# Kernel tuning notes

Hardware: AMD Instinct MI355X
Metric: run time of the kernel (lower is better)

Reference implementation:

```python
import jax, jax.numpy as jnp
import numpy as np

K = 20
EPS = 1e-5
SLOPE = 0.2


def _knn_idx(x, k):
    # x: [B, C, N] -> idx [B, N, k] of nearest neighbors by squared L2
    sq = jnp.sum(x * x, axis=1)                      # [B, N]
    inner = jnp.einsum('bcn,bcm->bnm', x, x)         # [B, N, N]
    neg_dist = 2.0 * inner - sq[:, :, None] - sq[:, None, :]
    return jax.lax.top_k(neg_dist, k)[1]             # [B, N, k]


def _edge_block(x, W, gamma, beta, k):
    # x: [B, C, N]; W: [O, 2C]; returns [B, O, N]
    idx = _knn_idx(x, k)
    xt = jnp.transpose(x, (0, 2, 1))                 # [B, N, C]
    nb = jax.vmap(lambda t, i: t[i])(xt, idx)        # [B, N, k, C] gather
    ctr = xt[:, :, None, :]
    edge = jnp.concatenate(
        [nb - ctr, jnp.broadcast_to(ctr, nb.shape)], axis=-1)  # [B, N, k, 2C]
    y = jnp.einsum('bnkc,oc->bonk', edge, W)         # 1x1 conv
    # BatchNorm2d (training mode: batch stats over B,N,k per channel)
    m = jnp.mean(y, axis=(0, 2, 3), keepdims=True)
    v = jnp.var(y, axis=(0, 2, 3), keepdims=True)
    y = (y - m) * jax.lax.rsqrt(v + EPS)
    y = y * gamma[None, :, None, None] + beta[None, :, None, None]
    y = jnp.where(y >= 0, y, SLOPE * y)              # LeakyReLU(0.2)
    return jnp.max(y, axis=-1)                       # max over k neighbors


def setup_inputs() -> dict:
    key = jax.random.key(0)
    ks = jax.random.split(key, 8)
    B, N = 8, 2048
    x = jax.random.normal(ks[0], (B, N, 3), dtype=jnp.float32)
    W1 = jax.random.normal(ks[1], (64, 6), dtype=jnp.float32) * 0.2
    W2 = jax.random.normal(ks[2], (128, 128), dtype=jnp.float32) * 0.08
    W3 = jax.random.normal(ks[3], (256, 256), dtype=jnp.float32) * 0.06
    g1, b1 = jnp.ones((64,), jnp.float32), jnp.zeros((64,), jnp.float32)
    g2, b2 = jnp.ones((128,), jnp.float32), jnp.zeros((128,), jnp.float32)
    g3, b3 = jnp.ones((256,), jnp.float32), jnp.zeros((256,), jnp.float32)
    L1 = jax.random.normal(ks[4], (1024, 448), dtype=jnp.float32) * 0.04
    L2 = jax.random.normal(ks[5], (2500, 1024), dtype=jnp.float32) * 0.03
    return {"x": x, "W1": W1, "g1": g1, "b1": b1, "W2": W2, "g2": g2,
            "b2": b2, "W3": W3, "g3": g3, "b3": b3, "L1": L1, "L2": L2}


def reference(x, W1, g1, b1, W2, g2, b2, W3, g3, b3, L1, L2):
    xT = jnp.transpose(x, (0, 2, 1))                 # [B, 3, N]
    x1 = _edge_block(xT, W1, g1, b1, K)              # [B, 64, N]
    x2 = _edge_block(x1, W2, g2, b2, K)              # [B, 128, N]
    x3 = _edge_block(x2, W3, g3, b3, K)              # [B, 256, N]
    feat = jnp.concatenate([x1, x2, x3], axis=1)     # [B, 448, N]
    pooled = jnp.max(feat, axis=-1)                  # adaptive_max_pool1d(1)
    h = pooled @ L1.T
    h = jnp.where(h >= 0, h, SLOPE * h)              # LeakyReLU(0.2)
    # dropout is identity in eval mode
    return h @ L2.T                                  # [B, 2500]
```

## Files before the change

kernel.cpp:

```cpp
#include <hip/hip_runtime.h>
#include <hip/hip_bf16.h>
#include <float.h>

#define K_NN 20
#define EPS 1e-5f
#define SLOPE 0.2f
constexpr int Bsz = 8;
constexpr int Npts = 2048;
constexpr int NQ = 8;
constexpr int BN = Bsz * Npts;

typedef __attribute__((ext_vector_type(8))) short short8v;
typedef __attribute__((ext_vector_type(4))) float f32x4;

__device__ __forceinline__ float dot4(float4 a, float4 b) {
  return a.x*b.x + a.y*b.y + a.z*b.z + a.w*b.w;
}
__device__ __forceinline__ unsigned encf(float f) {
  unsigned u = __float_as_uint(f);
  return (u & 0x80000000u) ? ~u : (u | 0x80000000u);
}
__device__ __forceinline__ float decf(unsigned e) {
  unsigned u = (e & 0x80000000u) ? (e & 0x7fffffffu) : ~e;
  return __uint_as_float(u);
}
__device__ __forceinline__ unsigned short f2bf(float x) {
  unsigned u = __float_as_uint(x);
  unsigned r = (u + 0x7fffu + ((u >> 16) & 1u)) >> 16;
  return (unsigned short)r;
}
__device__ __forceinline__ float bf2f(unsigned short h) {
  return __uint_as_float((unsigned)h << 16);
}
__device__ __forceinline__ f32x4 mfma16(short8v a, short8v b, f32x4 c) {
  return __builtin_amdgcn_mfma_f32_16x16x32_bf16(a, b, c, 0, 0, 0);
}

template<int C>
__global__ __launch_bounds__(256) void sq_kernel(const float* __restrict__ xt,
                                                 float* __restrict__ sq) {
  int p = blockIdx.x * 256 + threadIdx.x;
  if (p >= BN) return;
  const float* r = xt + (size_t)p * C;
  float s = 0.f;
  if constexpr (C % 4 == 0) {
    for (int c4 = 0; c4 < C / 4; ++c4) { float4 v = *(const float4*)(r + c4 * 4); s += dot4(v, v); }
  } else {
    #pragma unroll
    for (int c = 0; c < C; ++c) { float v = r[c]; s += v * v; }
  }
  sq[p] = s;
}

template<int C, int MT>
__global__ __launch_bounds__(256) void knn_part(const float* __restrict__ xt,
    const float* __restrict__ sq, float* __restrict__ pval, int* __restrict__ pidx) {
  constexpr int MQ = Npts / NQ;
  __shared__ __align__(16) float chk[MT][C];
  __shared__ float csq[MT];
  const int t = threadIdx.x, w = t >> 6, l = t & 63;
  const int rowblk = blockIdx.x / NQ;
  const int q = blockIdx.x - rowblk * NQ;
  const int p0 = rowblk * 256;
  const int b = p0 / Npts;
  const int myrow = p0 + w * 64 + l;

  float cr[C];
  #pragma unroll
  for (int c = 0; c < C; ++c) cr[c] = xt[(size_t)myrow * C + c];
  const float sqn = sq[myrow];

  float vals[K_NN]; int ids[K_NN];
  #pragma unroll
  for (int i = 0; i < K_NN; ++i) { vals[i] = -FLT_MAX; ids[i] = 0; }

  const int mbase = q * MQ;
  for (int m0 = mbase; m0 < mbase + MQ; m0 += MT) {
    __syncthreads();
    const float* s2 = xt + ((size_t)b * Npts + m0) * C;
    for (int e = t; e < MT * C; e += 256) chk[e / C][e - (e / C) * C] = s2[e];
    for (int e = t; e < MT; e += 256) csq[e] = sq[b * Npts + m0 + e];
    __syncthreads();
    for (int j = 0; j < MT; ++j) {
      float dt = 0.f;
      #pragma unroll
      for (int c = 0; c < C; ++c) dt += cr[c] * chk[j][c];
      float nd = 2.f * dt - sqn - csq[j];
      if (nd > vals[K_NN - 1]) {
        vals[K_NN - 1] = nd; ids[K_NN - 1] = m0 + j;
        #pragma unroll
        for (int i = K_NN - 1; i >= 1; --i) {
          if (vals[i] > vals[i - 1]) {
            float tv = vals[i]; vals[i] = vals[i-1]; vals[i-1] = tv;
            int ti = ids[i]; ids[i] = ids[i-1]; ids[i-1] = ti;
          }
        }
      }
    }
  }
  size_t base = ((size_t)q * BN + myrow) * K_NN;
  #pragma unroll
  for (int i = 0; i < K_NN; ++i) { pval[base + i] = vals[i]; pidx[base + i] = ids[i]; }
}

template<int NQM>
__global__ __launch_bounds__(256) void knn_merge(const float* __restrict__ pval,
    const int* __restrict__ pidx, int* __restrict__ idxout) {
  int p = blockIdx.x * 256 + threadIdx.x;
  if (p >= BN) return;
  float vals[K_NN]; int ids[K_NN];
  size_t base = (size_t)p * K_NN;
  #pragma unroll
  for (int i = 0; i < K_NN; ++i) { vals[i] = pval[base + i]; ids[i] = pidx[base + i]; }
  #pragma unroll
  for (int q = 1; q < NQM; ++q) {
    size_t b2 = ((size_t)q * BN + p) * K_NN;
    #pragma unroll
    for (int i = 0; i < K_NN; ++i) {
      float v = pval[b2 + i];
      if (v <= vals[K_NN - 1]) break;
      int m = pidx[b2 + i];
      vals[K_NN - 1] = v; ids[K_NN - 1] = m;
      #pragma unroll
      for (int r = K_NN - 1; r >= 1; --r) {
        if (vals[r] > vals[r - 1]) {
          float tv = vals[r]; vals[r] = vals[r-1]; vals[r-1] = tv;
          int ti = ids[r]; ids[r] = ids[r-1]; ids[r-1] = ti;
        }
      }
    }
  }
  int* op = idxout + (size_t)p * K_NN;
  #pragma unroll
  for (int i = 0; i < K_NN; ++i) op[i] = ids[i];
}

template<int C>
__global__ __launch_bounds__(256) void knn_fused(
    const unsigned short* __restrict__ xh, const unsigned short* __restrict__ xl,
    const float* __restrict__ sq, float* __restrict__ pval, int* __restrict__ pidx) {
  constexpr int KS = C / 32;
  constexpr int TPW = 4;
  __shared__ __align__(16) char smem[4 * 64 * 17 * 4];
  float (*dist)[64][17] = (float(*)[64][17])smem;
  float (*svv)[16][K_NN] = (float(*)[16][K_NN])smem;
  int   (*sii)[16][K_NN] = (int(*)[16][K_NN])(smem + 4 * 16 * K_NN * 4);
  const int bid = blockIdx.x;
  const int b = bid >> 8;
  const int rem = bid & 255;
  const int qt = rem >> 1, h = rem & 1;
  const int q0 = qt * 16;
  const int t = threadIdx.x, wv = t >> 6, l = t & 63, l15 = l & 15, grp = l >> 4;
  const unsigned short* xbh = xh + (size_t)b * Npts * C;
  const unsigned short* xbl = xl + (size_t)b * Npts * C;
  const float* sqb = sq + b * Npts;
  const int qi = q0 + l15;

  short8v bh[KS], bl[KS];
  #pragma unroll
  for (int ks = 0; ks < KS; ++ks) {
    const size_t a = (size_t)qi * C + ks * 32 + grp * 8;
    bh[ks] = *(const short8v*)(xbh + a);
    bl[ks] = *(const short8v*)(xbl + a);
  }
  const float sqn = sqb[qi];

  float vals[K_NN]; int ids[K_NN];
  #pragma unroll
  for (int i = 0; i < K_NN; ++i) { vals[i] = -FLT_MAX; ids[i] = 0; }

  #pragma unroll 1
  for (int ti = 0; ti < TPW; ++ti) {
    const int m0 = h * 1024 + (wv * TPW + ti) * 64;
    f32x4 acc[4];
    #pragma unroll
    for (int rt = 0; rt < 4; ++rt) acc[rt] = (f32x4){0.f, 0.f, 0.f, 0.f};
    #pragma unroll
    for (int ks = 0; ks < KS; ++ks) {
      #pragma unroll
      for (int rt = 0; rt < 4; ++rt) {
        const size_t aoff = (size_t)(m0 + rt * 16 + l15) * C + ks * 32 + grp * 8;
        const short8v a_h = *(const short8v*)(xbh + aoff);
        const short8v a_l = *(const short8v*)(xbl + aoff);
        acc[rt] = mfma16(a_h, bh[ks], acc[rt]);
        acc[rt] = mfma16(a_l, bh[ks], acc[rt]);
        acc[rt] = mfma16(a_h, bl[ks], acc[rt]);
      }
    }
    #pragma unroll
    for (int rt = 0; rt < 4; ++rt) {
      const int cb = m0 + rt * 16 + grp * 4;
      const float4 s4 = *(const float4*)(sqb + cb);
      const float sv[4] = {s4.x, s4.y, s4.z, s4.w};
      #pragma unroll
      for (int r = 0; r < 4; ++r) {
        const int cand = cb + r;
        float v = 2.f * acc[rt][r] - sqn - sv[r];
        if (cand == qi) v = 0.f;
        dist[wv][rt * 16 + grp * 4 + r][l15] = v;
      }
    }
    asm volatile("s_waitcnt lgkmcnt(0)" ::: "memory");
    __builtin_amdgcn_sched_barrier(0);
    #pragma unroll 4
    for (int j = 0; j < 16; ++j) {
      const float v = dist[wv][grp * 16 + j][l15];
      if (v > vals[K_NN - 1]) {
        const int cand = m0 + grp * 16 + j;
        vals[K_NN - 1] = v; ids[K_NN - 1] = cand;
        #pragma unroll
        for (int i = K_NN - 1; i >= 1; --i) {
          if (vals[i] > vals[i - 1]) {
            float tv = vals[i]; vals[i] = vals[i-1]; vals[i-1] = tv;
            int ti2 = ids[i]; ids[i] = ids[i-1]; ids[i-1] = ti2;
          }
        }
      }
    }
  }

  #pragma unroll
  for (int s2 = 1; s2 < 4; ++s2) {
    float ov[K_NN]; int oi[K_NN];
    #pragma unroll
    for (int i = 0; i < K_NN; ++i) {
      ov[i] = __shfl(vals[i], s2 * 16 + l15);
      oi[i] = __shfl(ids[i],  s2 * 16 + l15);
    }
    if (grp == 0) {
      #pragma unroll
      for (int i = 0; i < K_NN; ++i) {
        const float v = ov[i];
        if (v <= vals[K_NN - 1]) break;
        vals[K_NN - 1] = v; ids[K_NN - 1] = oi[i];
        #pragma unroll
        for (int r = K_NN - 1; r >= 1; --r) {
          if (vals[r] > vals[r - 1]) {
            float tv = vals[r]; vals[r] = vals[r-1]; vals[r-1] = tv;
            int ti2 = ids[r]; ids[r] = ids[r-1]; ids[r-1] = ti2;
          }
        }
      }
    }
  }
  __syncthreads();
  if (grp == 0) {
    #pragma unroll
    for (int i = 0; i < K_NN; ++i) { svv[wv][l15][i] = vals[i]; sii[wv][l15][i] = ids[i]; }
  }
  __syncthreads();
  if (t < 16) {
    #pragma unroll
    for (int s2 = 1; s2 < 4; ++s2) {
      #pragma unroll
      for (int i = 0; i < K_NN; ++i) {
        const float v = svv[s2][t][i];
        if (v <= vals[K_NN - 1]) break;
        vals[K_NN - 1] = v; ids[K_NN - 1] = sii[s2][t][i];
        #pragma unroll
        for (int r = K_NN - 1; r >= 1; --r) {
          if (vals[r] > vals[r - 1]) {
            float tv = vals[r]; vals[r] = vals[r-1]; vals[r-1] = tv;
            int ti2 = ids[r]; ids[r] = ids[r-1]; ids[r-1] = ti2;
          }
        }
      }
    }
    size_t base = ((size_t)h * BN + b * Npts + q0 + t) * K_NN;
    #pragma unroll
    for (int i = 0; i < K_NN; ++i) { pval[base + i] = vals[i]; pidx[base + i] = ids[i]; }
  }
}

template<int C, int O>
__global__ __launch_bounds__(256) void prep_w(const float* __restrict__ W,
    unsigned short* __restrict__ wh, unsigned short* __restrict__ wl) {
  int i = blockIdx.x * 256 + threadIdx.x;
  if (i >= 2 * O * C) return;
  int j = i / C, c = i - j * C;
  float v = (j < O) ? W[(size_t)j * 2 * C + c]
                    : (W[(size_t)(j - O) * 2 * C + C + c] - W[(size_t)(j - O) * 2 * C + c]);
  unsigned short h = f2bf(v);
  wh[i] = h; wl[i] = f2bf(v - bf2f(h));
}

template<int C, int N2>
__global__ __launch_bounds__(256) void zgemm(
    const unsigned short* __restrict__ xh, const unsigned short* __restrict__ xl,
    const unsigned short* __restrict__ wh, const unsigned short* __restrict__ wl,
    float* __restrict__ Z, int r0) {
  constexpr int KS = C / 32;
  constexpr int CB = N2 / 64;
  const int nb = blockIdx.x / CB, cb = blockIdx.x - nb * CB;
  const int ln0 = nb * 64;
  const int t = threadIdx.x, l = t & 63, wv = t >> 6, l15 = l & 15, grp = l >> 4;
  const int col = cb * 64 + wv * 16 + l15;
  f32x4 acc[4];
  #pragma unroll
  for (int rt = 0; rt < 4; ++rt) acc[rt] = (f32x4){0.f, 0.f, 0.f, 0.f};
  #pragma unroll
  for (int ks = 0; ks < KS; ++ks) {
    const int krd = ks * 32 + grp * 8;
    const short8v bh = *(const short8v*)(wh + (size_t)col * C + krd);
    const short8v bl = *(const short8v*)(wl + (size_t)col * C + krd);
    #pragma unroll
    for (int rt = 0; rt < 4; ++rt) {
      const size_t arow = (size_t)(r0 + ln0 + rt * 16 + l15) * C + krd;
      const short8v a_h = *(const short8v*)(xh + arow);
      const short8v a_l = *(const short8v*)(xl + arow);
      acc[rt] = mfma16(a_h, bh, acc[rt]);
      acc[rt] = mfma16(a_l, bh, acc[rt]);
      acc[rt] = mfma16(a_h, bl, acc[rt]);
    }
  }
  #pragma unroll
  for (int rt = 0; rt < 4; ++rt)
    #pragma unroll
    for (int r = 0; r < 4; ++r)
      Z[(size_t)(ln0 + rt * 16 + grp * 4 + r) * N2 + col] = acc[rt][r];
}

template<int O, int NPP>
__global__ __launch_bounds__(256) void nbr_reduce(
    const float* __restrict__ Z, const int* __restrict__ idx,
    float* __restrict__ mx, float* __restrict__ mn,
    float* __restrict__ psum, float* __restrict__ psq, int r0) {
  constexpr int PPB = 256 / O;
  constexpr int O2 = 2 * O;
  const int t = threadIdx.x;
  const int o = t % O;
  const int sub = t / O;
  float ls = 0.f, lq = 0.f;
  for (int it = 0; it < NPP / PPB; ++it) {
    const int p = r0 + blockIdx.x * NPP + it * PPB + sub;
    const int bbase = (p >> 11) << 11;
    const int* ip = idx + (size_t)p * K_NN;
    const float base = Z[(size_t)(p - r0) * O2 + O + o];
    float vmx = -FLT_MAX, vmn = FLT_MAX;
    #pragma unroll
    for (int k = 0; k < K_NN; ++k) {
      const int nbrow = bbase + ip[k] - r0;
      const float y = Z[(size_t)nbrow * O2 + o] + base;
      ls += y; lq = fmaf(y, y, lq);
      vmx = fmaxf(vmx, y); vmn = fminf(vmn, y);
    }
    mx[(size_t)p * O + o] = vmx;
    mn[(size_t)p * O + o] = vmn;
  }
  if constexpr (PPB > 1) {
    __shared__ float s1[256], s2[256];
    s1[t] = ls; s2[t] = lq;
    __syncthreads();
    if (sub == 0) {
      psum[(size_t)blockIdx.x * O + o] = ls + s1[t + O];
      psq [(size_t)blockIdx.x * O + o] = lq + s2[t + O];
    }
  } else {
    psum[(size_t)blockIdx.x * O + o] = ls;
    psq [(size_t)blockIdx.x * O + o] = lq;
  }
}

template<int C, int O, int G, int NPG, int CPT>
__global__ __launch_bounds__(256) void edge_kernel(const float* __restrict__ xt,
    const int* __restrict__ idx, const float* __restrict__ W,
    float* __restrict__ mx, float* __restrict__ mn,
    float* __restrict__ psum, float* __restrict__ psq) {
  constexpr int WP = O / (64 * CPT);
  constexpr int TPB = 64 * WP * NPG;
  constexpr int PPG = G / NPG;
  static_assert(TPB == 256, "block must be 256 threads");
  __shared__ __align__(16) float pts[G][K_NN + 1][C];
  __shared__ int ids[G][K_NN + 1];
  __shared__ float shps[NPG][O];
  __shared__ float shpq[NPG][O];
  const int t = threadIdx.x;
  const int p0 = blockIdx.x * G;
  const int b = p0 / Npts;

  for (int e = t; e < G * (K_NN + 1); e += TPB) {
    int g = e / (K_NN + 1), j = e - g * (K_NN + 1);
    ids[g][j] = (j == 0) ? (p0 + g) : (b * Npts + idx[(size_t)(p0 + g) * K_NN + (j - 1)]);
  }
  __syncthreads();
  for (int e = t; e < G * (K_NN + 1) * C; e += TPB) {
    int g = e / ((K_NN + 1) * C), rem = e - g * ((K_NN + 1) * C);
    int j = rem / C, c = rem - j * C;
    pts[g][j][c] = xt[(size_t)ids[g][j] * C + c];
  }
  __syncthreads();

  const int w = t >> 6, l = t & 63;
  const int pg = w / WP, wp = w - pg * WP;
  const int o0 = wp * 64 + l;
  float ls0 = 0.f, lq0 = 0.f;

  for (int it = 0; it < PPG; ++it) {
    const int g = pg * PPG + it;
    float yk0[K_NN];
    float u0 = 0.f, v0 = 0.f;
    #pragma unroll
    for (int k = 0; k < K_NN; ++k) yk0[k] = 0.f;
    const float* W0 = W + (size_t)o0 * (2 * C);
    #pragma unroll
    for (int c = 0; c < C; ++c) {
      const float wl = W0[c], whv = W0[C + c], ccv = pts[g][0][c];
      u0 += wl * ccv; v0 += whv * ccv;
      #pragma unroll
      for (int k = 0; k < K_NN; ++k) yk0[k] += wl * pts[g][k + 1][c];
    }
    const int n = p0 + g - b * Npts;
    const size_t obase = ((size_t)b * Npts + n) * O;
    const float base = v0 - u0;
    float vmx = -FLT_MAX, vmn = FLT_MAX;
    #pragma unroll
    for (int k = 0; k < K_NN; ++k) {
      float y = yk0[k] + base;
      ls0 += y; lq0 += y * y;
      vmx = fmaxf(vmx, y); vmn = fminf(vmn, y);
    }
    mx[obase + o0] = vmx; mn[obase + o0] = vmn;
  }

  shps[pg][o0] = ls0; shpq[pg][o0] = lq0;
  __syncthreads();
  if (t < O) {
    float s = 0.f, qq = 0.f;
    #pragma unroll
    for (int i = 0; i < NPG; ++i) { s += shps[i][t]; qq += shpq[i][t]; }
    psum[(size_t)blockIdx.x * O + t] = s;
    psq [(size_t)blockIdx.x * O + t] = qq;
  }
}

template<int O, int NBLK>
__global__ __launch_bounds__(256) void stats_part(const float* __restrict__ psum,
    const float* __restrict__ psq, double* __restrict__ pp, double* __restrict__ pq) {
  constexpr int NS = 16;
  constexpr int SL = NBLK / NS;
  const int l = threadIdx.x & 63, w = threadIdx.x >> 6;
  const int os = blockIdx.x % (O / 64), sl = blockIdx.x / (O / 64);
  const int o = os * 64 + l;
  double s = 0.0, ss = 0.0;
  for (int i = sl * SL + w; i < (sl + 1) * SL; i += 4) {
    s  += (double)psum[(size_t)i * O + o];
    ss += (double)psq [(size_t)i * O + o];
  }
  __shared__ double sh[2][4][64];
  sh[0][w][l] = s; sh[1][w][l] = ss;
  __syncthreads();
  if (w == 0) {
    s  = sh[0][0][l] + sh[0][1][l] + sh[0][2][l] + sh[0][3][l];
    ss = sh[1][0][l] + sh[1][1][l] + sh[1][2][l] + sh[1][3][l];
    pp[(size_t)sl * O + o] = s;
    pq[(size_t)sl * O + o] = ss;
  }
}

template<int O>
__global__ __launch_bounds__(64) void stats_final(const double* __restrict__ pp,
    const double* __restrict__ pq,
    const float* __restrict__ gamma, const float* __restrict__ beta,
    float* __restrict__ scale, float* __restrict__ bias) {
  const int o = blockIdx.x * 64 + threadIdx.x;
  double s = 0.0, ss = 0.0;
  #pragma unroll
  for (int sl = 0; sl < 16; ++sl) { s += pp[(size_t)sl * O + o]; ss += pq[(size_t)sl * O + o]; }
  double cnt = (double)Bsz * Npts * K_NN;
  double m = s / cnt;
  double var = ss / cnt - m * m;
  float g = gamma[o];
  float sc = g * rsqrtf((float)var + EPS);
  scale[o] = sc;
  bias[o] = beta[o] - (float)m * sc;
}

__global__ __launch_bounds__(256) void reset_pool(unsigned* __restrict__ pooled) {
  int i = blockIdx.x * 256 + threadIdx.x;
  if (i < Bsz * 448) pooled[i] = 0u;
}

template<int O, int COFF, bool WNC>
__global__ __launch_bounds__(256) void apply_kernel(const float* __restrict__ mx,
    const float* __restrict__ mn, const float* __restrict__ scale,
    const float* __restrict__ bias, float* __restrict__ xnc,
    unsigned short* __restrict__ xh, unsigned short* __restrict__ xl,
    unsigned* __restrict__ pooled) {
  constexpr int OT = O / 64;
  constexpr int NCH = Npts / 256;
  const int bid = blockIdx.x;
  const int nchunk = bid % NCH;
  const int ot = (bid / NCH) % OT;
  const int b = bid / (NCH * OT);
  const int l = threadIdx.x & 63, w = threadIdx.x >> 6;
  const int o = ot * 64 + l;
  const float sc = scale[o], bs = bias[o];
  const bool pos = (sc >= 0.f);
  float vmax = -FLT_MAX;
  const int n0 = nchunk * 256;
  for (int i = 0; i < 64; ++i) {
    int n = n0 + w + i * 4;
    size_t ix = ((size_t)b * Npts + n) * O + o;
    float raw = pos ? mx[ix] : mn[ix];
    float y = raw * sc + bs;
    y = (y >= 0.f) ? y : SLOPE * y;
    if constexpr (WNC) {
      xnc[ix] = y;
      unsigned short h = f2bf(y);
      xh[ix] = h;
      xl[ix] = f2bf(y - bf2f(h));
    }
    vmax = fmaxf(vmax, y);
  }
  __shared__ float sh[4][64];
  sh[w][l] = vmax;
  __syncthreads();
  if (w == 0) {
    float m = fmaxf(fmaxf(sh[0][l], sh[1][l]), fmaxf(sh[2][l], sh[3][l]));
    atomicMax(pooled + b * 448 + COFF + o, encf(m));
  }
}

template<int CIN, bool LRELU, bool DECODE>
__global__ __launch_bounds__(64) void fc_kernel(const void* __restrict__ inv,
    const float* __restrict__ Wt, float* __restrict__ out, int JO) {
  int j = blockIdx.x;
  const float* wr = Wt + (size_t)j * CIN;
  float acc[Bsz];
  #pragma unroll
  for (int b = 0; b < Bsz; ++b) acc[b] = 0.f;
  for (int c = threadIdx.x; c < CIN; c += 64) {
    float wv = wr[c];
    #pragma unroll
    for (int b = 0; b < Bsz; ++b) {
      float x;
      if constexpr (DECODE) x = decf(((const unsigned*)inv)[b * CIN + c]);
      else                  x = ((const float*)inv)[b * CIN + c];
      acc[b] += x * wv;
    }
  }
  #pragma unroll
  for (int b = 0; b < Bsz; ++b) {
    float v = acc[b];
    #pragma unroll
    for (int w = 32; w > 0; w >>= 1) v += __shfl_down(v, w);
    if (threadIdx.x == 0) {
      if (LRELU) v = (v >= 0.f) ? v : SLOPE * v;
      out[b * JO + j] = v;
    }
  }
}

extern "C" void kernel_launch(void* const* d_in, const int* in_sizes, int n_in,
                              void* d_out, int out_size, void* d_ws, size_t ws_size,
                              hipStream_t stream) {
  const float* x   = (const float*)d_in[0];
  const float* W1  = (const float*)d_in[1];
  const float* g1  = (const float*)d_in[2];
  const float* b1  = (const float*)d_in[3];
  const float* W2  = (const float*)d_in[4];
  const float* g2  = (const float*)d_in[5];
  const float* b2  = (const float*)d_in[6];
  const float* W3  = (const float*)d_in[7];
  const float* g3  = (const float*)d_in[8];
  const float* b3  = (const float*)d_in[9];
  const float* L1  = (const float*)d_in[10];
  const float* L2  = (const float*)d_in[11];
  float* out = (float*)d_out;

  float* ws = (float*)d_ws;
  size_t off = 0;
  float* sq    = ws + off; off += BN;
  int*   idxb  = (int*)(ws + off); off += (size_t)BN * K_NN;
  float* mx    = ws + off; off += (size_t)BN * 256;
  float* mn    = ws + off; off += (size_t)BN * 256;
  float* Z     = ws + off; off += (size_t)BN * 256;
  float* psum  = ws + off; off += (size_t)2048 * 256;
  float* psq   = ws + off; off += (size_t)2048 * 256;
  off = (off + 1) & ~(size_t)1;
  double* pp   = (double*)(ws + off); off += 16 * 256 * 2;
  double* pq   = (double*)(ws + off); off += 16 * 256 * 2;
  float* scale = ws + off; off += 256;
  float* bias  = ws + off; off += 256;
  float* x1nc  = ws + off; off += (size_t)BN * 64;
  float* x2nc  = ws + off; off += (size_t)BN * 128;
  unsigned short* xh1 = (unsigned short*)(ws + off); off += (size_t)BN * 64 / 2;
  unsigned short* xl1 = (unsigned short*)(ws + off); off += (size_t)BN * 64 / 2;
  unsigned short* xh2 = (unsigned short*)(ws + off); off += (size_t)BN * 128 / 2;
  unsigned short* xl2 = (unsigned short*)(ws + off); off += (size_t)BN * 128 / 2;
  unsigned* pooled = (unsigned*)(ws + off); off += Bsz * 448;
  float* h     = ws + off; off += Bsz * 1024;
  unsigned short* wch2 = (unsigned short*)(ws + off); off += 256 * 64 / 2;
  unsigned short* wcl2 = (unsigned short*)(ws + off); off += 256 * 64 / 2;
  unsigned short* wch3 = (unsigned short*)(ws + off); off += 512 * 128 / 2;
  unsigned short* wcl3 = (unsigned short*)(ws + off); off += 512 * 128 / 2;
  float* pval = mx;
  int*   pidx = (int*)mn;

  reset_pool<<<14, 256, 0, stream>>>(pooled);
  prep_w<64, 128><<<(2 * 128 * 64 + 255) / 256, 256, 0, stream>>>(W2, wch2, wcl2);
  prep_w<128, 256><<<(2 * 256 * 128 + 255) / 256, 256, 0, stream>>>(W3, wch3, wcl3);

  sq_kernel<3><<<64, 256, 0, stream>>>(x, sq);
  knn_part<3, 64><<<(BN / 256) * NQ, 256, 0, stream>>>(x, sq, pval, pidx);
  knn_merge<NQ><<<64, 256, 0, stream>>>(pval, pidx, idxb);
  edge_kernel<3, 64, 16, 4, 1><<<BN / 16, 256, 0, stream>>>(x, idxb, W1, mx, mn, psum, psq);
  stats_part<64, 1024><<<16, 256, 0, stream>>>(psum, psq, pp, pq);
  stats_final<64><<<1, 64, 0, stream>>>(pp, pq, g1, b1, scale, bias);
  apply_kernel<64, 0, true><<<64, 256, 0, stream>>>(mx, mn, scale, bias, x1nc, xh1, xl1, pooled);

  sq_kernel<64><<<64, 256, 0, stream>>>(x1nc, sq);
  knn_fused<64><<<Bsz * 256, 256, 0, stream>>>(xh1, xl1, sq, pval, pidx);
  knn_merge<2><<<64, 256, 0, stream>>>(pval, pidx, idxb);
  zgemm<64, 256><<<(BN / 64) * 4, 256, 0, stream>>>(xh1, xl1, wch2, wcl2, Z, 0);
  nbr_reduce<128, 16><<<BN / 16, 256, 0, stream>>>(Z, idxb, mx, mn, psum, psq, 0);
  stats_part<128, 1024><<<32, 256, 0, stream>>>(psum, psq, pp, pq);
  stats_final<128><<<2, 64, 0, stream>>>(pp, pq, g2, b2, scale, bias);
  apply_kernel<128, 64, true><<<128, 256, 0, stream>>>(mx, mn, scale, bias, x2nc, xh2, xl2, pooled);

  sq_kernel<128><<<64, 256, 0, stream>>>(x2nc, sq);
  knn_fused<128><<<Bsz * 256, 256, 0, stream>>>(xh2, xl2, sq, pval, pidx);
  knn_merge<2><<<64, 256, 0, stream>>>(pval, pidx, idxb);
  for (int pass = 0; pass < 2; ++pass) {
    const int r0 = pass * (BN / 2);
    zgemm<128, 512><<<(BN / 2 / 64) * 8, 256, 0, stream>>>(xh2, xl2, wch3, wcl3, Z, r0);
    nbr_reduce<256, 8><<<BN / 2 / 8, 256, 0, stream>>>(Z, idxb, mx, mn,
        psum + (size_t)pass * 1024 * 256, psq + (size_t)pass * 1024 * 256, r0);
  }
  stats_part<256, 2048><<<64, 256, 0, stream>>>(psum, psq, pp, pq);
  stats_final<256><<<4, 64, 0, stream>>>(pp, pq, g3, b3, scale, bias);
  apply_kernel<256, 192, false><<<256, 256, 0, stream>>>(mx, mn, scale, bias, nullptr, nullptr, nullptr, pooled);

  fc_kernel<448, true, true><<<1024, 64, 0, stream>>>(pooled, L1, h, 1024);
  fc_kernel<1024, false, false><<<2500, 64, 0, stream>>>(h, L2, out, 2500);
}
```

Baseline: 1.028 ms.

## Replace per-lane insertion-sort top-k with radix bisection threshold selection in fused kNN

The fused kNN kernel keeps all 64 encoded distances per lane in registers. It then finds the 20th-largest key per query with a 32-step bitwise bisection, using counts summed across the four lane groups by shuffles. Candidates above the threshold are compacted into shared memory with atomics, and ties are resolved by lowest index. A small bubble sort and a cross-wave merge follow. This replaces the branchy, divergent insertion sort over each candidate, but adds 64 live registers per thread, 32 serial counting passes, and shared-memory atomics.

After: 1.033 ms. About the same (+0.5%).

```diff
diff --git a/kernel.cpp b/kernel.cpp
--- a/kernel.cpp
+++ b/kernel.cpp
@@ -136,42 +136,42 @@
 }
 
 template<int C>
-__global__ __launch_bounds__(256) void knn_fused(
+__global__ __launch_bounds__(256) void knn_bisect(
     const unsigned short* __restrict__ xh, const unsigned short* __restrict__ xl,
     const float* __restrict__ sq, float* __restrict__ pval, int* __restrict__ pidx) {
   constexpr int KS = C / 32;
-  constexpr int TPW = 4;
-  __shared__ __align__(16) char smem[4 * 64 * 17 * 4];
-  float (*dist)[64][17] = (float(*)[64][17])smem;
-  float (*svv)[16][K_NN] = (float(*)[16][K_NN])smem;
-  int   (*sii)[16][K_NN] = (int(*)[16][K_NN])(smem + 4 * 16 * K_NN * 4);
+  constexpr int CAP = 32;
+  __shared__ unsigned okey[4][16][K_NN];
+  __shared__ unsigned short oidx[4][16][K_NN];
+  __shared__ unsigned short bbuf[4][16][CAP];
+  __shared__ unsigned ocnt[4][16], bct[4][16];
   const int bid = blockIdx.x;
   const int b = bid >> 8;
   const int rem = bid & 255;
   const int qt = rem >> 1, h = rem & 1;
   const int q0 = qt * 16;
+  const int cbase = h * 1024;
   const int t = threadIdx.x, wv = t >> 6, l = t & 63, l15 = l & 15, grp = l >> 4;
   const unsigned short* xbh = xh + (size_t)b * Npts * C;
   const unsigned short* xbl = xl + (size_t)b * Npts * C;
   const float* sqb = sq + b * Npts;
   const int qi = q0 + l15;
 
-  short8v bh[KS], bl[KS];
+  if (l < 16) { ocnt[wv][l] = 0u; bct[wv][l] = 0u; }
+
+  short8v qh[KS], qlo[KS];
   #pragma unroll
   for (int ks = 0; ks < KS; ++ks) {
     const size_t a = (size_t)qi * C + ks * 32 + grp * 8;
-    bh[ks] = *(const short8v*)(xbh + a);
-    bl[ks] = *(const short8v*)(xbl + a);
+    qh[ks]  = *(const short8v*)(xbh + a);
+    qlo[ks] = *(const short8v*)(xbl + a);
   }
   const float sqn = sqb[qi];
 
-  float vals[K_NN]; int ids[K_NN];
-  #pragma unroll
-  for (int i = 0; i < K_NN; ++i) { vals[i] = -FLT_MAX; ids[i] = 0; }
-
-  #pragma unroll 1
-  for (int ti = 0; ti < TPW; ++ti) {
-    const int m0 = h * 1024 + (wv * TPW + ti) * 64;
+  unsigned keys[64];
+  #pragma unroll
+  for (int ti = 0; ti < 4; ++ti) {
+    const int m0 = cbase + wv * 256 + ti * 64;
     f32x4 acc[4];
     #pragma unroll
     for (int rt = 0; rt < 4; ++rt) acc[rt] = (f32x4){0.f, 0.f, 0.f, 0.f};
@@ -182,9 +182,9 @@
         const size_t aoff = (size_t)(m0 + rt * 16 + l15) * C + ks * 32 + grp * 8;
         const short8v a_h = *(const short8v*)(xbh + aoff);
         const short8v a_l = *(const short8v*)(xbl + aoff);
-        acc[rt] = mfma16(a_h, bh[ks], acc[rt]);
-        acc[rt] = mfma16(a_l, bh[ks], acc[rt]);
-        acc[rt] = mfma16(a_h, bl[ks], acc[rt]);
+        acc[rt] = mfma16(a_h, qh[ks], acc[rt]);
+        acc[rt] = mfma16(a_l, qh[ks], acc[rt]);
+        acc[rt] = mfma16(a_h, qlo[ks], acc[rt]);
       }
     }
     #pragma unroll
@@ -194,81 +194,101 @@
       const float sv[4] = {s4.x, s4.y, s4.z, s4.w};
       #pragma unroll
       for (int r = 0; r < 4; ++r) {
-        const int cand = cb + r;
         float v = 2.f * acc[rt][r] - sqn - sv[r];
-        if (cand == qi) v = 0.f;
-        dist[wv][rt * 16 + grp * 4 + r][l15] = v;
+        if (cb + r == qi) v = 0.f;
+        keys[ti * 16 + rt * 4 + r] = encf(v);
       }
     }
-    asm volatile("s_waitcnt lgkmcnt(0)" ::: "memory");
-    __builtin_amdgcn_sched_barrier(0);
-    #pragma unroll 4
-    for (int j = 0; j < 16; ++j) {
-      const float v = dist[wv][grp * 16 + j][l15];
-      if (v > vals[K_NN - 1]) {
-        const int cand = m0 + grp * 16 + j;
-        vals[K_NN - 1] = v; ids[K_NN - 1] = cand;
+  }
+
+  unsigned L = 0u;
+  #pragma unroll 1
+  for (int bit = 31; bit >= 0; --bit) {
+    const unsigned X = L | (1u << bit);
+    int c0 = 0, c1 = 0, c2 = 0, c3 = 0;
+    #pragma unroll
+    for (int j = 0; j < 64; j += 4) {
+      c0 += (keys[j + 0] >= X) ? 1 : 0;
+      c1 += (keys[j + 1] >= X) ? 1 : 0;
+      c2 += (keys[j + 2] >= X) ? 1 : 0;
+      c3 += (keys[j + 3] >= X) ? 1 : 0;
+    }
+    int c = (c0 + c1) + (c2 + c3);
+    c += __shfl_xor(c, 16);
+    c += __shfl_xor(c, 32);
+    if (c >= K_NN) L = X;
+  }
+
+  __syncthreads();
+  #pragma unroll
+  for (int j = 0; j < 64; ++j) {
+    const unsigned k = keys[j];
+    const int cloc = wv * 256 + (j >> 4) * 64 + ((j >> 2) & 3) * 16 + grp * 4 + (j & 3);
+    if (k > L) {
+      unsigned s = atomicAdd(&ocnt[wv][l15], 1u);
+      okey[wv][l15][s] = k;
+      oidx[wv][l15][s] = (unsigned short)cloc;
+    } else if (k == L) {
+      unsigned p = atomicAdd(&bct[wv][l15], 1u);
+      if (p < CAP) bbuf[wv][l15][p] = (unsigned short)cloc;
+    }
+  }
+  __syncthreads();
+
+  if (grp == 0) {
+    const int q = l15;
+    const unsigned above = ocnt[wv][q];
+    const unsigned need = K_NN - above;
+    const unsigned m = min(bct[wv][q], (unsigned)CAP);
+    for (unsigned i2 = 0; i2 < need; ++i2) {
+      unsigned best = 0xFFFFu; int bj = 0;
+      for (unsigned j2 = 0; j2 < m; ++j2) {
+        unsigned ii = bbuf[wv][q][j2];
+        if (ii < best) { best = ii; bj = (int)j2; }
+      }
+      okey[wv][q][above + i2] = L;
+      oidx[wv][q][above + i2] = (unsigned short)best;
+      bbuf[wv][q][bj] = 0xFFFFu;
+    }
+    for (int i2 = 0; i2 < K_NN - 1; ++i2)
+      for (int j2 = 0; j2 < K_NN - 1 - i2; ++j2) {
+        unsigned ka = okey[wv][q][j2], kb = okey[wv][q][j2 + 1];
+        unsigned short ia = oidx[wv][q][j2], ib = oidx[wv][q][j2 + 1];
+        if (kb > ka || (kb == ka && ib < ia)) {
+          okey[wv][q][j2] = kb; okey[wv][q][j2 + 1] = ka;
+          oidx[wv][q][j2] = ib; oidx[wv][q][j2 + 1] = ia;
+        }
+      }
+  }
+  __syncthreads();
+
+  if (t < 16) {
+    unsigned kv[K_NN]; int iv[K_NN];
+    #pragma unroll
+    for (int i = 0; i < K_NN; ++i) { kv[i] = okey[0][t][i]; iv[i] = oidx[0][t][i]; }
+    #pragma unroll
+    for (int s2 = 1; s2 < 4; ++s2) {
+      #pragma unroll
+      for (int i = 0; i < K_NN; ++i) {
+        const unsigned k = okey[s2][t][i];
+        if (k <= kv[K_NN - 1]) break;
+        const int ii = oidx[s2][t][i];
+        kv[K_NN - 1] = k; iv[K_NN - 1] = ii;
         #pragma unroll
-        for (int i = K_NN - 1; i >= 1; --i) {
-          if (vals[i] > vals[i - 1]) {
-            float tv = vals[i]; vals[i] = vals[i-1]; vals[i-1] = tv;
-            int ti2 = ids[i]; ids[i] = ids[i-1]; ids[i-1] = ti2;
+        for (int r = K_NN - 1; r >= 1; --r) {
+          if (kv[r] > kv[r - 1]) {
+            unsigned tk = kv[r]; kv[r] = kv[r-1]; kv[r-1] = tk;
+            int ti2 = iv[r]; iv[r] = iv[r-1]; iv[r-1] = ti2;
           }
         }
       }
     }
-  }
-
-  #pragma unroll
-  for (int s2 = 1; s2 < 4; ++s2) {
-    float ov[K_NN]; int oi[K_NN];
+    size_t base = ((size_t)h * BN + b * Npts + q0 + t) * K_NN;
     #pragma unroll
     for (int i = 0; i < K_NN; ++i) {
-      ov[i] = __shfl(vals[i], s2 * 16 + l15);
-      oi[i] = __shfl(ids[i],  s2 * 16 + l15);
-    }
-    if (grp == 0) {
-      #pragma unroll
-      for (int i = 0; i < K_NN; ++i) {
-        const float v = ov[i];
-        if (v <= vals[K_NN - 1]) break;
-        vals[K_NN - 1] = v; ids[K_NN - 1] = oi[i];
-        #pragma unroll
-        for (int r = K_NN - 1; r >= 1; --r) {
-          if (vals[r] > vals[r - 1]) {
-            float tv = vals[r]; vals[r] = vals[r-1]; vals[r-1] = tv;
-            int ti2 = ids[r]; ids[r] = ids[r-1]; ids[r-1] = ti2;
-          }
-        }
-      }
-    }
-  }
-  __syncthreads();
-  if (grp == 0) {
-    #pragma unroll
-    for (int i = 0; i < K_NN; ++i) { svv[wv][l15][i] = vals[i]; sii[wv][l15][i] = ids[i]; }
-  }
-  __syncthreads();
-  if (t < 16) {
-    #pragma unroll
-    for (int s2 = 1; s2 < 4; ++s2) {
-      #pragma unroll
-      for (int i = 0; i < K_NN; ++i) {
-        const float v = svv[s2][t][i];
-        if (v <= vals[K_NN - 1]) break;
-        vals[K_NN - 1] = v; ids[K_NN - 1] = sii[s2][t][i];
-        #pragma unroll
-        for (int r = K_NN - 1; r >= 1; --r) {
-          if (vals[r] > vals[r - 1]) {
-            float tv = vals[r]; vals[r] = vals[r-1]; vals[r-1] = tv;
-            int ti2 = ids[r]; ids[r] = ids[r-1]; ids[r-1] = ti2;
-          }
-        }
-      }
-    }
-    size_t base = ((size_t)h * BN + b * Npts + q0 + t) * K_NN;
-    #pragma unroll
-    for (int i = 0; i < K_NN; ++i) { pval[base + i] = vals[i]; pidx[base + i] = ids[i]; }
+      pval[base + i] = decf(kv[i]);
+      pidx[base + i] = cbase + iv[i];
+    }
   }
 }
 
@@ -610,7 +630,7 @@
   apply_kernel<64, 0, true><<<64, 256, 0, stream>>>(mx, mn, scale, bias, x1nc, xh1, xl1, pooled);
 
   sq_kernel<64><<<64, 256, 0, stream>>>(x1nc, sq);
-  knn_fused<64><<<Bsz * 256, 256, 0, stream>>>(xh1, xl1, sq, pval, pidx);
+  knn_bisect<64><<<Bsz * 256, 256, 0, stream>>>(xh1, xl1, sq, pval, pidx);
   knn_merge<2><<<64, 256, 0, stream>>>(pval, pidx, idxb);
   zgemm<64, 256><<<(BN / 64) * 4, 256, 0, stream>>>(xh1, xl1, wch2, wcl2, Z, 0);
   nbr_reduce<128, 16><<<BN / 16, 256, 0, stream>>>(Z, idxb, mx, mn, psum, psq, 0);
@@ -619,7 +639,7 @@
   apply_kernel<128, 64, true><<<128, 256, 0, stream>>>(mx, mn, scale, bias, x2nc, xh2, xl2, pooled);
 
   sq_kernel<128><<<64, 256, 0, stream>>>(x2nc, sq);
-  knn_fused<128><<<Bsz * 256, 256, 0, stream>>>(xh2, xl2, sq, pval, pidx);
+  knn_bisect<128><<<Bsz * 256, 256, 0, stream>>>(xh2, xl2, sq, pval, pidx);
   knn_merge<2><<<64, 256, 0, stream>>>(pval, pidx, idxb);
   for (int pass = 0; pass < 2; ++pass) {
     const int r0 = pass * (BN / 2);
```
